# Optimization experiments

Hardware: AMD Instinct MI355X
Metric: run time of the kernel (lower is better)

## Reference

```python
import jax, jax.numpy as jnp
import numpy as np

B, S, E, H = 4, 2048, 1024, 16
D = E // H  # head dim = 64


def setup_inputs() -> dict:
    key = jax.random.key(0)
    ks = jax.random.split(key, 5)
    scale = 0.02
    return {
        "x": jax.random.normal(ks[0], (B, S, E), dtype=jnp.float32),
        "Wa_w": jax.random.normal(ks[1], (3 * E, E), dtype=jnp.float32) * scale,
        "Wa_b": jax.random.normal(ks[2], (3 * E,), dtype=jnp.float32) * scale,
        "Wo_w": jax.random.normal(ks[3], (E, E), dtype=jnp.float32) * scale,
        "Wo_b": jax.random.normal(ks[4], (E,), dtype=jnp.float32) * scale,
    }


def reference(x, Wa_w, Wa_b, Wo_w, Wo_b):
    b, s, e = x.shape
    # Fused QKV projection (torch Linear: x @ W^T + b)
    qkv = jnp.einsum("bse,fe->bsf", x, Wa_w) + Wa_b  # [B,S,3E]
    q, k, v = jnp.split(qkv, 3, axis=-1)
    # [B,S,E] -> [B,H,S,D]
    def heads(t):
        return t.reshape(b, s, H, D).transpose(0, 2, 1, 3)
    q, k, v = heads(q), heads(k), heads(v)
    # Causal attention with explicit score matrix (as in the original)
    scores = jnp.einsum("bhqd,bhkd->bhqk", q, k) / jnp.sqrt(jnp.float32(D))
    causal = jnp.tril(jnp.ones((s, s), dtype=bool))
    scores = jnp.where(causal, scores, -jnp.inf)
    attn = jax.nn.softmax(scores, axis=-1)  # dropout p=0 -> identity
    out = jnp.einsum("bhqk,bhkd->bhqd", attn, v)  # [B,H,S,D]
    out = out.transpose(0, 2, 1, 3).reshape(b, s, e)
    return jnp.einsum("bse,fe->bsf", out, Wo_w) + Wo_b
```

## Files before the change

### kernel.cpp

```cpp
#include <hip/hip_runtime.h>
#include <hip/hip_bf16.h>
#include <cstdint>

typedef __bf16 bf16_t;
typedef __attribute__((ext_vector_type(8))) __bf16 bf16x8;
typedef __attribute__((ext_vector_type(4))) __bf16 bf16x4;
typedef __attribute__((ext_vector_type(4))) float f32x4;

#define B_ 4
#define S_ 2048
#define E_ 1024
#define H_ 16
#define D_ 64

#define QSCALE 0.18033688011112042f

__global__ void cvt_all(const float* __restrict__ x, const float* __restrict__ wa,
                        const float* __restrict__ wo,
                        bf16_t* __restrict__ xb, bf16_t* __restrict__ wab,
                        bf16_t* __restrict__ wob) {
    constexpr int N1 = (B_ * S_ * E_) / 4;
    constexpr int N2 = (3 * E_ * E_) / 4;
    constexpr int N3 = (E_ * E_) / 4;
    int i = blockIdx.x * blockDim.x + threadIdx.x;
    int stride = gridDim.x * blockDim.x;
    for (; i < N1 + N2 + N3; i += stride) {
        const float* src; bf16_t* dst; int k;
        if (i < N1) { src = x; dst = xb; k = i; }
        else if (i < N1 + N2) { src = wa; dst = wab; k = i - N1; }
        else { src = wo; dst = wob; k = i - N1 - N2; }
        f32x4 v = reinterpret_cast<const f32x4*>(src)[k];
        bf16x4 o;
        o.x = (bf16_t)v.x; o.y = (bf16_t)v.y; o.z = (bf16_t)v.z; o.w = (bf16_t)v.w;
        reinterpret_cast<bf16x4*>(dst)[k] = o;
    }
}

__device__ __forceinline__ void gload_lds16(const bf16_t* g, bf16_t* l) {
    __builtin_amdgcn_global_load_lds((const __attribute__((address_space(1))) void*)g,
                                     (__attribute__((address_space(3))) void*)l, 16, 0, 0);
}

__device__ __forceinline__ void wait_vm4() { asm volatile("s_waitcnt vmcnt(4)" ::: "memory"); }
__device__ __forceinline__ void wait_vm0() { asm volatile("s_waitcnt vmcnt(0)" ::: "memory"); }

__device__ __forceinline__ int fragOffG(int row, int kc) {
    const int line = row >> 1;
    const int ch = ((row & 1) << 2) | kc;
    return line * 64 + ((ch ^ (line & 7)) << 3);
}

__launch_bounds__(256, 3)
__global__ void gemm_qkv(const bf16_t* __restrict__ A, const bf16_t* __restrict__ Bm,
                         const float* __restrict__ bias,
                         bf16_t* __restrict__ Qg, bf16_t* __restrict__ Kg,
                         bf16_t* __restrict__ Vtg) {
    constexpr int K = 1024, BK = 32;
    constexpr int BM = 128, BN = 128;
    __shared__ __align__(16) bf16_t As[3][BM * BK];
    __shared__ __align__(16) bf16_t Bs[3][BN * BK];

    constexpr int NG = 12;
    const int xcd = blockIdx.x & 7;
    const int u = blockIdx.x >> 3;
    const int grp = 4 * NG;
    const int g = u / grp, r2 = u % grp;
    const int ntl = r2 >> 2, q = r2 & 3;
    const int mt0 = xcd * 8 + q;
    const int nt = g * NG + ntl;
    const int m0a = mt0 * BM, m0b = (mt0 + 4) * BM, n0 = nt * BN;

    const int t = threadIdx.x;
    const int lane = t & 63;
    const int wid = t >> 6;
    const int wr = wid >> 1, wc = wid & 1;
    const int lr = lane & 15, lg = lane >> 4;

    auto mkSrc = [&](const bf16_t* base, int c, int row0) {
        const int line = c >> 3, chg = (c & 7) ^ (line & 7);
        return base + (int64_t)(row0 + 2 * line + (chg >> 2)) * K + (chg & 3) * 8;
    };
    const bf16_t* aSrcA0 = mkSrc(A, t, m0a);
    const bf16_t* aSrcA1 = mkSrc(A, t + 256, m0a);
    const bf16_t* aSrcB0 = mkSrc(A, t, m0b);
    const bf16_t* aSrcB1 = mkSrc(A, t + 256, m0b);
    const bf16_t* bSrc0 = mkSrc(Bm, t, n0);
    const bf16_t* bSrc1 = mkSrc(Bm, t + 256, n0);

    auto stageT = [&](int v, int buf) {
        const int kt = v & 31;
        const bf16_t* a0 = (v < 32) ? aSrcA0 : aSrcB0;
        const bf16_t* a1 = (v < 32) ? aSrcA1 : aSrcB1;
        gload_lds16(a0 + kt * BK, &As[buf][t * 8]);
        gload_lds16(a1 + kt * BK, &As[buf][(t + 256) * 8]);
        gload_lds16(bSrc0 + kt * BK, &Bs[buf][t * 8]);
        gload_lds16(bSrc1 + kt * BK, &Bs[buf][(t + 256) * 8]);
    };

    f32x4 acc[4][4] = {};

    float bv[4];
#pragma unroll
    for (int j = 0; j < 4; ++j) bv[j] = bias[n0 + wc * 64 + j * 16 + lr];

    auto epi = [&](int m0) {
        const int which = n0 >> 10;
        const int h = (((n0 & 1023) + wc * 64) >> 6);
#pragma unroll
        for (int i = 0; i < 4; ++i) {
#pragma unroll
            for (int r = 0; r < 4; ++r) {
                const int m = m0 + wr * 64 + i * 16 + lg * 4 + r;
                const int b = m >> 11, si = m & (S_ - 1);
                if (which == 0) {
                    bf16_t* p = &Qg[(((int64_t)(b * H_ + h)) * S_ + si) * D_ + lr];
#pragma unroll
                    for (int j = 0; j < 4; ++j)
                        p[j * 16] = (bf16_t)((acc[i][j][r] + bv[j]) * QSCALE);
                } else if (which == 1) {
                    bf16_t* p = &Kg[(((int64_t)(b * H_ + h)) * S_ + si) * D_ + lr];
#pragma unroll
                    for (int j = 0; j < 4; ++j)
                        p[j * 16] = (bf16_t)(acc[i][j][r] + bv[j]);
                } else {
                    bf16_t* p = &Vtg[(((int64_t)(b * H_ + h)) * D_ + lr) * S_ + si];
#pragma unroll
                    for (int j = 0; j < 4; ++j)
                        p[(int64_t)(j * 16) * S_] = (bf16_t)(acc[i][j][r] + bv[j]);
                }
            }
        }
    };

    auto body = [&](int bufc) {
        bf16x8 bfr[4], afr[4];
#pragma unroll
        for (int j = 0; j < 4; ++j)
            bfr[j] = *(const bf16x8*)&Bs[bufc][fragOffG(wc * 64 + j * 16 + lr, lg)];
#pragma unroll
        for (int i = 0; i < 4; ++i)
            afr[i] = *(const bf16x8*)&As[bufc][fragOffG(wr * 64 + i * 16 + lr, lg)];
#pragma unroll
        for (int i = 0; i < 4; ++i)
#pragma unroll
            for (int j = 0; j < 4; ++j)
                acc[i][j] = __builtin_amdgcn_mfma_f32_16x16x32_bf16(afr[i], bfr[j], acc[i][j], 0, 0, 0);
    };

    stageT(0, 0);
    stageT(1, 1);

    int bufc = 0, bufs = 2;
    for (int v = 0; v < 32; ++v) {
        wait_vm4();
        __builtin_amdgcn_s_barrier();
        __builtin_amdgcn_sched_barrier(0);
        stageT(v + 2, bufs);
        body(bufc);
        bufc = (bufc == 2) ? 0 : bufc + 1;
        bufs = (bufs == 2) ? 0 : bufs + 1;
    }
    epi(m0a);
#pragma unroll
    for (int i = 0; i < 4; ++i)
#pragma unroll
        for (int j = 0; j < 4; ++j)
            acc[i][j] = f32x4{0.f, 0.f, 0.f, 0.f};

    for (int v = 32; v < 64; ++v) {
        if (v < 63) wait_vm4(); else wait_vm0();
        __builtin_amdgcn_s_barrier();
        __builtin_amdgcn_sched_barrier(0);
        if (v + 2 < 64) stageT(v + 2, bufs);
        body(bufc);
        bufc = (bufc == 2) ? 0 : bufc + 1;
        bufs = (bufs == 2) ? 0 : bufs + 1;
    }
    epi(m0b);
}

__launch_bounds__(256, 3)
__global__ void gemm_proj(const bf16_t* __restrict__ A, const bf16_t* __restrict__ Bm,
                          const float* __restrict__ bias, float* __restrict__ Outf) {
    constexpr int K = 1024, BK = 32, NKT = K / BK;
    constexpr int BM = 128, BN = 128, N = 1024, NG = 8;
    __shared__ __align__(16) bf16_t As[3][BM * BK];
    __shared__ __align__(16) bf16_t Bs[3][BN * BK];

    const int xcd = blockIdx.x & 7;
    const int u = blockIdx.x >> 3;
    const int grp = 8 * NG;
    const int g = u / grp, r2 = u % grp;
    const int ntl = r2 / 8, mtl = r2 & 7;
    const int mt = xcd * 8 + mtl;
    const int nt = g * NG + ntl;
    const int m0 = mt * BM, n0 = nt * BN;

    const int t = threadIdx.x;
    const int lane = t & 63;
    const int wid = t >> 6;
    const int wr = wid >> 1, wc = wid & 1;
    const int lr = lane & 15, lg = lane >> 4;

    auto mkSrc = [&](const bf16_t* base, int c, int row0) {
        const int line = c >> 3, chg = (c & 7) ^ (line & 7);
        return base + (int64_t)(row0 + 2 * line + (chg >> 2)) * K + (chg & 3) * 8;
    };
    const bf16_t* aSrc0 = mkSrc(A, t, m0);
    const bf16_t* aSrc1 = mkSrc(A, t + 256, m0);
    const bf16_t* bSrc0 = mkSrc(Bm, t, n0);
    const bf16_t* bSrc1 = mkSrc(Bm, t + 256, n0);

    auto stageT = [&](int kt, int buf) {
        gload_lds16(aSrc0 + kt * BK, &As[buf][t * 8]);
        gload_lds16(aSrc1 + kt * BK, &As[buf][(t + 256) * 8]);
        gload_lds16(bSrc0 + kt * BK, &Bs[buf][t * 8]);
        gload_lds16(bSrc1 + kt * BK, &Bs[buf][(t + 256) * 8]);
    };

    f32x4 acc[4][4] = {};

    stageT(0, 0);
    stageT(1, 1);

    int bufc = 0, bufs = 2;
    for (int kt = 0; kt < NKT; ++kt) {
        if (kt < NKT - 1) wait_vm4(); else wait_vm0();
        __builtin_amdgcn_s_barrier();
        __builtin_amdgcn_sched_barrier(0);

        if (kt + 2 < NKT) stageT(kt + 2, bufs);

        bf16x8 bfr[4], afr[4];
#pragma unroll
        for (int j = 0; j < 4; ++j)
            bfr[j] = *(const bf16x8*)&Bs[bufc][fragOffG(wc * 64 + j * 16 + lr, lg)];
#pragma unroll
        for (int i = 0; i < 4; ++i)
            afr[i] = *(const bf16x8*)&As[bufc][fragOffG(wr * 64 + i * 16 + lr, lg)];

#pragma unroll
        for (int i = 0; i < 4; ++i)
#pragma unroll
            for (int j = 0; j < 4; ++j)
                acc[i][j] = __builtin_amdgcn_mfma_f32_16x16x32_bf16(afr[i], bfr[j], acc[i][j], 0, 0, 0);

        bufc = (bufc == 2) ? 0 : bufc + 1;
        bufs = (bufs == 2) ? 0 : bufs + 1;
    }

    float bv[4];
#pragma unroll
    for (int j = 0; j < 4; ++j) bv[j] = bias[n0 + wc * 64 + j * 16 + lr];
#pragma unroll
    for (int i = 0; i < 4; ++i) {
#pragma unroll
        for (int r = 0; r < 4; ++r) {
            const int m = m0 + wr * 64 + i * 16 + lg * 4 + r;
            float* p = &Outf[(int64_t)m * N + n0 + wc * 64 + lr];
#pragma unroll
            for (int j = 0; j < 4; ++j)
                p[j * 16] = acc[i][j][r] + bv[j];
        }
    }
}

__launch_bounds__(256, 4)
__global__ void attn_causal(const bf16_t* __restrict__ Qg, const bf16_t* __restrict__ Kg,
                            const bf16_t* __restrict__ Vtg, bf16_t* __restrict__ Og) {
    __shared__ __align__(16) bf16_t Ks[2][64 * 64];
    __shared__ __align__(16) bf16_t Vs[2][64 * 64];
    __shared__ __align__(16) bf16_t P_lds[4][16 * 64];

    const int bid = blockIdx.x;
    const int xcd = bid & 7, j = bid >> 3;
    const int bh = (j >> 4) * 8 + xcd;
    const int i = j & 15;
    const int qtA = i, qtB = 31 - i;

    const int t = threadIdx.x, lane = t & 63, w = t >> 6;
    const int lr = lane & 15, lg = lane >> 4;
    const int q0A = qtA * 64 + w * 16;
    const int q0B = qtB * 64 + w * 16;

    const bf16_t* Qb = Qg + (int64_t)bh * S_ * D_;
    const bf16_t* Kb = Kg + (int64_t)bh * S_ * D_;
    const bf16_t* Vb = Vtg + (int64_t)bh * D_ * S_;

    const int srow = t >> 3;
    const int scol_sw = (t & 7) ^ (srow & 7);

    auto stageK = [&](int buf, int kv0) {
        const bf16_t* base = Kb + (kv0 + srow) * D_ + scol_sw * 8;
        gload_lds16(base, &Ks[buf][t * 8]);
        gload_lds16(base + 32 * D_, &Ks[buf][t * 8 + 2048]);
    };
    auto stageV = [&](int buf, int kv0) {
        const bf16_t* base = Vb + srow * S_ + kv0 + scol_sw * 8;
        gload_lds16(base, &Vs[buf][t * 8]);
        gload_lds16(base + 32 * S_, &Vs[buf][t * 8 + 2048]);
    };

    auto psw = [](int row, int col) {
        return row * 64 + ((((col >> 3) ^ (row & 7)) << 3) | (col & 7));
    };

    bf16x8 qfA[2], qfB[2];
#pragma unroll
    for (int kk = 0; kk < 2; ++kk) {
        qfA[kk] = *(const bf16x8*)&Qb[(q0A + lr) * D_ + kk * 32 + lg * 8];
        qfB[kk] = *(const bf16x8*)&Qb[(q0B + lr) * D_ + kk * 32 + lg * 8];
    }

    bf16x8 ones;
#pragma unroll
    for (int e = 0; e < 8; ++e) ones[e] = (bf16_t)1.0f;

    f32x4 oA[4] = {}, oB[4] = {};
    f32x4 lA = {}, lB = {};

    int cur = 0;
    stageK(0, 0);
    stageV(0, 0);
    __syncthreads();

    for (int tkv = 0; tkv <= qtB; ++tkv) {
        const int kv0 = tkv * 64;
        if (tkv < qtB) { stageK(cur ^ 1, kv0 + 64); stageV(cur ^ 1, kv0 + 64); }

        auto process = [&](int q0, const bf16x8* qf, f32x4* o, f32x4& accl, bf16_t* Pw) {
            f32x4 sc[4] = {};
            __builtin_amdgcn_s_setprio(1);
#pragma unroll
            for (int nj = 0; nj < 4; ++nj) {
                if (kv0 + nj * 16 <= q0 + 15) {
                    const int krow = nj * 16 + lr;
#pragma unroll
                    for (int kk = 0; kk < 2; ++kk) {
                        bf16x8 kfr = *(const bf16x8*)&Ks[cur][krow * 64 + (((kk * 4 + lg) ^ (krow & 7)) * 8)];
                        sc[nj] = __builtin_amdgcn_mfma_f32_16x16x32_bf16(qf[kk], kfr, sc[nj], 0, 0, 0);
                    }
                }
            }
            __builtin_amdgcn_s_setprio(0);

            if (kv0 + 64 > q0) {
#pragma unroll
                for (int nj = 0; nj < 4; ++nj) {
                    const int col = kv0 + nj * 16 + lr;
#pragma unroll
                    for (int r = 0; r < 4; ++r) {
                        const int rowg = q0 + lg * 4 + r;
                        if (col > rowg) sc[nj][r] = -1e30f;
                    }
                }
            }

#pragma unroll
            for (int nj = 0; nj < 4; ++nj)
#pragma unroll
                for (int r = 0; r < 4; ++r)
                    Pw[psw(lg * 4 + r, nj * 16 + lr)] = (bf16_t)__builtin_amdgcn_exp2f(sc[nj][r]);
            asm volatile("s_waitcnt lgkmcnt(0)" ::: "memory");
            __builtin_amdgcn_sched_barrier(0);

            __builtin_amdgcn_s_setprio(1);
#pragma unroll
            for (int kk = 0; kk < 2; ++kk) {
                bf16x8 pa = *(const bf16x8*)&Pw[psw(lr, kk * 32 + lg * 8)];
                accl = __builtin_amdgcn_mfma_f32_16x16x32_bf16(pa, ones, accl, 0, 0, 0);
#pragma unroll
                for (int nd = 0; nd < 4; ++nd) {
                    const int vrow = nd * 16 + lr;
                    bf16x8 vf = *(const bf16x8*)&Vs[cur][vrow * 64 + (((kk * 4 + lg) ^ (vrow & 7)) * 8)];
                    o[nd] = __builtin_amdgcn_mfma_f32_16x16x32_bf16(pa, vf, o[nd], 0, 0, 0);
                }
            }
            __builtin_amdgcn_s_setprio(0);
        };

        process(q0B, qfB, oB, lB, &P_lds[w][0]);
        if (tkv <= qtA) process(q0A, qfA, oA, lA, &P_lds[w][0]);

        __syncthreads();
        cur ^= 1;
    }

    const int b = bh >> 4, h = bh & 15;
#pragma unroll
    for (int r = 0; r < 4; ++r) {
        const float rlA = 1.0f / lA[r];
        const float rlB = 1.0f / lB[r];
        const int rA = q0A + lg * 4 + r;
        const int rB = q0B + lg * 4 + r;
#pragma unroll
        for (int nd = 0; nd < 4; ++nd) {
            Og[((int64_t)(b * S_ + rA)) * E_ + h * D_ + nd * 16 + lr] = (bf16_t)(oA[nd][r] * rlA);
            Og[((int64_t)(b * S_ + rB)) * E_ + h * D_ + nd * 16 + lr] = (bf16_t)(oB[nd][r] * rlB);
        }
    }
}

extern "C" void kernel_launch(void* const* d_in, const int* in_sizes, int n_in,
                              void* d_out, int out_size, void* d_ws, size_t ws_size,
                              hipStream_t stream) {
    const float* x    = (const float*)d_in[0];
    const float* Wa_w = (const float*)d_in[1];
    const float* Wa_b = (const float*)d_in[2];
    const float* Wo_w = (const float*)d_in[3];
    const float* Wo_b = (const float*)d_in[4];
    float* out = (float*)d_out;

    const size_t M = (size_t)B_ * S_;
    char* ws = (char*)d_ws;
    bf16_t* xb  = (bf16_t*)ws; ws += M * E_ * 2;
    bf16_t* wab = (bf16_t*)ws; ws += (size_t)3 * E_ * E_ * 2;
    bf16_t* wob = (bf16_t*)ws; ws += (size_t)E_ * E_ * 2;
    bf16_t* Qg  = (bf16_t*)ws; ws += M * E_ * 2;
    bf16_t* Kg  = (bf16_t*)ws; ws += M * E_ * 2;
    bf16_t* Vtg = (bf16_t*)ws; ws += M * E_ * 2;
    bf16_t* Og  = (bf16_t*)ws; ws += M * E_ * 2;

    cvt_all<<<2048, 256, 0, stream>>>(x, Wa_w, Wo_w, xb, wab, wob);

    gemm_qkv<<<768, 256, 0, stream>>>(xb, wab, Wa_b, Qg, Kg, Vtg);

    attn_causal<<<B_ * H_ * 16, 256, 0, stream>>>(Qg, Kg, Vtg, Og);

    gemm_proj<<<512, 256, 0, stream>>>(Og, wob, Wo_b, out);
}
```

Before: 173.8 us.

## Make proj GEMM waves independent with private LDS tiles and no barriers

Restructures the output projection GEMM so each wave computes its own 64x64 tile with a private double-buffered LDS region, staging its own A and B slices. This removes the workgroup-wide s_barrier per k-step and the shared 128x128 tile, trading cross-wave data reuse for independence. Each wave now loads its full A and B slices, so global/L2 traffic per output roughly doubles, and LDS per block rises to 64KB, reducing occupancy (launch bound lowered to 2). The block-to-tile mapping is also changed.

```diff
diff --git a/kernel.cpp b/kernel.cpp
--- a/kernel.cpp
+++ b/kernel.cpp
@@ -42,6 +42,7 @@
 }
 
 __device__ __forceinline__ void wait_vm4() { asm volatile("s_waitcnt vmcnt(4)" ::: "memory"); }
+__device__ __forceinline__ void wait_vm8() { asm volatile("s_waitcnt vmcnt(8)" ::: "memory"); }
 __device__ __forceinline__ void wait_vm0() { asm volatile("s_waitcnt vmcnt(0)" ::: "memory"); }
 
 __device__ __forceinline__ int fragOffG(int row, int kc) {
@@ -179,43 +180,48 @@
     epi(m0b);
 }
 
-__launch_bounds__(256, 3)
+__launch_bounds__(256, 2)
 __global__ void gemm_proj(const bf16_t* __restrict__ A, const bf16_t* __restrict__ Bm,
                           const float* __restrict__ bias, float* __restrict__ Outf) {
     constexpr int K = 1024, BK = 32, NKT = K / BK;
-    constexpr int BM = 128, BN = 128, N = 1024, NG = 8;
-    __shared__ __align__(16) bf16_t As[3][BM * BK];
-    __shared__ __align__(16) bf16_t Bs[3][BN * BK];
-
-    const int xcd = blockIdx.x & 7;
-    const int u = blockIdx.x >> 3;
-    const int grp = 8 * NG;
-    const int g = u / grp, r2 = u % grp;
-    const int ntl = r2 / 8, mtl = r2 & 7;
-    const int mt = xcd * 8 + mtl;
-    const int nt = g * NG + ntl;
-    const int m0 = mt * BM, n0 = nt * BN;
+    constexpr int N = 1024;
+    __shared__ __align__(16) bf16_t WS[4 * 2 * 4096];
 
     const int t = threadIdx.x;
     const int lane = t & 63;
     const int wid = t >> 6;
-    const int wr = wid >> 1, wc = wid & 1;
     const int lr = lane & 15, lg = lane >> 4;
+
+    const int xcd = blockIdx.x & 7;
+    const int u = blockIdx.x >> 3;
+    const int nt = u & 15;
+    const int mtq = xcd * 4 + (u >> 4);
+    const int mt = mtq * 4 + wid;
+    const int m0 = mt * 64, n0 = nt * 64;
+
+    bf16_t* Aw = &WS[wid * 8192];
+    bf16_t* Bw = &WS[wid * 8192 + 2048];
 
     auto mkSrc = [&](const bf16_t* base, int c, int row0) {
         const int line = c >> 3, chg = (c & 7) ^ (line & 7);
         return base + (int64_t)(row0 + 2 * line + (chg >> 2)) * K + (chg & 3) * 8;
     };
-    const bf16_t* aSrc0 = mkSrc(A, t, m0);
-    const bf16_t* aSrc1 = mkSrc(A, t + 256, m0);
-    const bf16_t* bSrc0 = mkSrc(Bm, t, n0);
-    const bf16_t* bSrc1 = mkSrc(Bm, t + 256, n0);
+    const bf16_t* aS[4];
+    const bf16_t* bS[4];
+#pragma unroll
+    for (int i = 0; i < 4; ++i) {
+        aS[i] = mkSrc(A, lane + i * 64, m0);
+        bS[i] = mkSrc(Bm, lane + i * 64, n0);
+    }
 
     auto stageT = [&](int kt, int buf) {
-        gload_lds16(aSrc0 + kt * BK, &As[buf][t * 8]);
-        gload_lds16(aSrc1 + kt * BK, &As[buf][(t + 256) * 8]);
-        gload_lds16(bSrc0 + kt * BK, &Bs[buf][t * 8]);
-        gload_lds16(bSrc1 + kt * BK, &Bs[buf][(t + 256) * 8]);
+        bf16_t* a = Aw + buf * 4096;
+        bf16_t* b = Bw + buf * 4096;
+#pragma unroll
+        for (int i = 0; i < 4; ++i) {
+            gload_lds16(aS[i] + kt * BK, &a[(lane + i * 64) * 8]);
+            gload_lds16(bS[i] + kt * BK, &b[(lane + i * 64) * 8]);
+        }
     };
 
     f32x4 acc[4][4] = {};
@@ -223,41 +229,39 @@
     stageT(0, 0);
     stageT(1, 1);
 
-    int bufc = 0, bufs = 2;
     for (int kt = 0; kt < NKT; ++kt) {
-        if (kt < NKT - 1) wait_vm4(); else wait_vm0();
-        __builtin_amdgcn_s_barrier();
+        if (kt < NKT - 1) wait_vm8(); else wait_vm0();
+
+        const int bufc = kt & 1;
+        const bf16_t* a = Aw + bufc * 4096;
+        const bf16_t* b = Bw + bufc * 4096;
+
+        bf16x8 afr[4], bfr[4];
+#pragma unroll
+        for (int i = 0; i < 4; ++i) {
+            afr[i] = *(const bf16x8*)&a[fragOffG(i * 16 + lr, lg)];
+            bfr[i] = *(const bf16x8*)&b[fragOffG(i * 16 + lr, lg)];
+        }
+        asm volatile("s_waitcnt lgkmcnt(0)" ::: "memory");
         __builtin_amdgcn_sched_barrier(0);
-
-        if (kt + 2 < NKT) stageT(kt + 2, bufs);
-
-        bf16x8 bfr[4], afr[4];
-#pragma unroll
-        for (int j = 0; j < 4; ++j)
-            bfr[j] = *(const bf16x8*)&Bs[bufc][fragOffG(wc * 64 + j * 16 + lr, lg)];
-#pragma unroll
-        for (int i = 0; i < 4; ++i)
-            afr[i] = *(const bf16x8*)&As[bufc][fragOffG(wr * 64 + i * 16 + lr, lg)];
+        if (kt + 2 < NKT) stageT(kt + 2, bufc);
 
 #pragma unroll
         for (int i = 0; i < 4; ++i)
 #pragma unroll
             for (int j = 0; j < 4; ++j)
                 acc[i][j] = __builtin_amdgcn_mfma_f32_16x16x32_bf16(afr[i], bfr[j], acc[i][j], 0, 0, 0);
-
-        bufc = (bufc == 2) ? 0 : bufc + 1;
-        bufs = (bufs == 2) ? 0 : bufs + 1;
     }
 
     float bv[4];
 #pragma unroll
-    for (int j = 0; j < 4; ++j) bv[j] = bias[n0 + wc * 64 + j * 16 + lr];
+    for (int j = 0; j < 4; ++j) bv[j] = bias[n0 + j * 16 + lr];
 #pragma unroll
     for (int i = 0; i < 4; ++i) {
 #pragma unroll
         for (int r = 0; r < 4; ++r) {
-            const int m = m0 + wr * 64 + i * 16 + lg * 4 + r;
-            float* p = &Outf[(int64_t)m * N + n0 + wc * 64 + lr];
+            const int m = m0 + i * 16 + lg * 4 + r;
+            float* p = &Outf[(int64_t)m * N + n0 + lr];
 #pragma unroll
             for (int j = 0; j < 4; ++j)
                 p[j * 16] = acc[i][j][r] + bv[j];
```

Result: slower. 177.4 us (+2.1%).
